# Kernel tuning notes

Hardware: AMD Instinct MI355X
Metric: run time of the kernel (lower is better)

## Reference

```python
import jax, jax.numpy as jnp
import numpy as np

N = 100000   # total atoms in batch of graphs
E = 400000   # directed edges
B = 1024     # graphs / proteins in batch
F_XD = 78    # atom feature dim
DIM = 32     # GIN hidden dim
OUT_DIM = 128
EMB = 128    # protein token embed dim
VOCAB = 26   # num_features_xt + 1
NF = 32      # conv1d filters
SEQ = 1000
K = 8        # conv1d kernel size
LM = 1024    # LM embedding dim
FLAT = NF * (SEQ - K + 1)  # 31776
COMB = 2 * OUT_DIM + 2 * LM  # 2304


def setup_inputs() -> dict:
    key = jax.random.key(0)
    ks = jax.random.split(key, 40)
    s = 0.05  # weight scale
    nrm = lambda k, shape: (jax.random.normal(k, shape, jnp.float32) * s)
    inp = {
        'x': jax.random.normal(ks[0], (N, F_XD), jnp.float32),
        'edge_index': jax.random.randint(ks[1], (2, E), 0, N),
        'batch': jnp.sort(jax.random.randint(ks[2], (N,), 0, B)),
        'target': jax.random.randint(ks[3], (B, SEQ), 0, VOCAB),
        'drug_lm': jax.random.normal(ks[4], (B, LM), jnp.float32),
        'protein_lm': jax.random.normal(ks[5], (B, LM), jnp.float32),
        # GINConv 1 MLP (78->32->32)
        'w1a': nrm(ks[6], (F_XD, DIM)), 'b1a': jnp.zeros((DIM,), jnp.float32),
        'w1b': nrm(ks[7], (DIM, DIM)), 'b1b': jnp.zeros((DIM,), jnp.float32),
        # GINConv 2-5 MLPs stacked (32->32->32)
        'gw_a': nrm(ks[8], (4, DIM, DIM)), 'gb_a': jnp.zeros((4, DIM), jnp.float32),
        'gw_b': nrm(ks[9], (4, DIM, DIM)), 'gb_b': jnp.zeros((4, DIM), jnp.float32),
        # BatchNorm affine params for 5 layers
        'bn_gamma': jnp.ones((5, DIM), jnp.float32),
        'bn_beta': jnp.zeros((5, DIM), jnp.float32),
        'fc1_xd_w': nrm(ks[10], (DIM, OUT_DIM)), 'fc1_xd_b': jnp.zeros((OUT_DIM,), jnp.float32),
        'emb': nrm(ks[11], (VOCAB, EMB)),
        'convxt_w': nrm(ks[12], (NF, EMB, K)), 'convxt_b': jnp.zeros((NF,), jnp.float32),
        'fc1_xt_w': nrm(ks[13], (FLAT, OUT_DIM)) * 0.1, 'fc1_xt_b': jnp.zeros((OUT_DIM,), jnp.float32),
        'fc1_w': nrm(ks[14], (COMB, 1024)), 'fc1_b': jnp.zeros((1024,), jnp.float32),
        'fc2_w': nrm(ks[15], (1024, 256)), 'fc2_b': jnp.zeros((256,), jnp.float32),
        'out_w': nrm(ks[16], (256, 1)), 'out_b': jnp.zeros((1,), jnp.float32),
    }
    return inp


def reference(x, edge_index, batch, target, drug_lm, protein_lm,
              w1a, b1a, w1b, b1b, gw_a, gb_a, gw_b, gb_b,
              bn_gamma, bn_beta, fc1_xd_w, fc1_xd_b, emb,
              convxt_w, convxt_b, fc1_xt_w, fc1_xt_b,
              fc1_w, fc1_b, fc2_w, fc2_b, out_w, out_b):
    src, dst = edge_index[0], edge_index[1]

    def bn(z, g, be):
        mu = z.mean(axis=0)
        var = jnp.mean((z - mu) ** 2, axis=0)
        return g * (z - mu) * jax.lax.rsqrt(var + 1e-5) + be

    def gin(h, wa, ba, wb, bb, g, be):
        # GIN aggregation: out_i = MLP((1+eps)*x_i + sum_{j->i} x_j), eps=0
        agg = jax.ops.segment_sum(h[src], dst, num_segments=N)
        z = jnp.maximum((h + agg) @ wa + ba, 0.0) @ wb + bb
        return bn(jnp.maximum(z, 0.0), g, be)  # relu then BatchNorm

    h = gin(x, w1a, b1a, w1b, b1b, bn_gamma[0], bn_beta[0])
    for i in range(4):  # convs 2..5
        h = gin(h, gw_a[i], gb_a[i], gw_b[i], gb_b[i], bn_gamma[i + 1], bn_beta[i + 1])

    xg = jax.ops.segment_sum(h, batch, num_segments=B)  # global_add_pool -> [B, 32]
    xg = jnp.maximum(xg @ fc1_xd_w + fc1_xd_b, 0.0)      # [B, 128]

    e = emb[target]                      # [B, SEQ, EMB]
    e = jnp.transpose(e, (0, 2, 1))      # [B, EMB, SEQ]
    c = jax.lax.conv_general_dilated(e, convxt_w, (1,), 'VALID',
                                     dimension_numbers=('NCH', 'OIH', 'NCH'))
    c = jnp.maximum(c + convxt_b[None, :, None], 0.0)    # [B, 32, 993]
    xt = jnp.maximum(c.reshape(B, -1) @ fc1_xt_w + fc1_xt_b, 0.0)  # [B, 128]

    xc = jnp.concatenate([xg, xt, drug_lm, protein_lm], axis=1)  # [B, 2304]
    xc = jnp.maximum(xc @ fc1_w + fc1_b, 0.0)
    xc = jnp.maximum(xc @ fc2_w + fc2_b, 0.0)
    return xc @ out_w + out_b  # [B, 1]
```

## Files before the change

### kernel.cpp

```cpp
#include <hip/hip_runtime.h>
#include <hip/hip_bf16.h>

#define NN 100000
#define EE 400000
#define BB 1024
#define FXD 78
#define DIMC 32
#define VOCABN 26
#define SEQN 1000
#define PCONV 993
#define FLATN 31776
#define COMB 2304
#define NB_SC 391

static __device__ __forceinline__ float relu_(float x) { return x > 0.f ? x : 0.f; }

template<int KC, bool TRANSFORM>
__global__ __launch_bounds__(256) void gin_gemm1(
    const float* __restrict__ H, const float* __restrict__ W, float* __restrict__ P,
    const float* __restrict__ sums, const float* __restrict__ gamma, const float* __restrict__ beta)
{
    __shared__ float As[32][KC + 1];
    __shared__ float Ws[KC][32];
    __shared__ float scale_s[32], shift_s[32];
    const int tid = threadIdx.x;
    const int row0 = blockIdx.x * 32;
    if (TRANSFORM) {
        if (tid < 32) {
            float mu = sums[tid] * (1.f / NN);
            float var = sums[32 + tid] * (1.f / NN) - mu * mu;
            float rs = rsqrtf(var + 1e-5f);
            float a = gamma[tid] * rs;
            scale_s[tid] = a;
            shift_s[tid] = beta[tid] - mu * a;
        }
    }
    for (int idx = tid; idx < KC * 32; idx += 256) Ws[idx / 32][idx % 32] = W[idx];
    __syncthreads();
    for (int idx = tid; idx < 32 * KC; idx += 256) {
        int r = idx / KC, k = idx % KC;
        float v = H[(row0 + r) * KC + k];
        if (TRANSFORM) v = v * scale_s[k] + shift_s[k];
        As[r][k] = v;
    }
    __syncthreads();
    const int col = tid & 31, rg = tid >> 5;
    float acc[4] = {0.f, 0.f, 0.f, 0.f};
    for (int k = 0; k < KC; ++k) {
        float w = Ws[k][col];
#pragma unroll
        for (int r = 0; r < 4; ++r) acc[r] += As[rg + 8 * r][k] * w;
    }
#pragma unroll
    for (int r = 0; r < 4; ++r) P[(row0 + rg + 8 * r) * 32 + col] = acc[r];
}

__global__ __launch_bounds__(256) void gin_gemm2(
    const float* __restrict__ P, const float* __restrict__ AGG, const float* __restrict__ W,
    const float* __restrict__ ba, const float* __restrict__ bb,
    float* __restrict__ Y, float* __restrict__ partials)
{
    __shared__ float As[32][33];
    __shared__ float Ws[32][32];
    __shared__ float red[8][32], red2[8][32];
    const int tid = threadIdx.x;
    const int row0 = blockIdx.x * 32;
    for (int idx = tid; idx < 1024; idx += 256) Ws[idx / 32][idx % 32] = W[idx];
    for (int idx = tid; idx < 1024; idx += 256) {
        int r = idx / 32, k = idx % 32;
        int g = (row0 + r) * 32 + k;
        As[r][k] = relu_(P[g] + AGG[g] + ba[k]);
    }
    __syncthreads();
    const int col = tid & 31, rg = tid >> 5;
    float acc[4] = {0.f, 0.f, 0.f, 0.f};
    for (int k = 0; k < 32; ++k) {
        float w = Ws[k][col];
#pragma unroll
        for (int r = 0; r < 4; ++r) acc[r] += As[rg + 8 * r][k] * w;
    }
    float s = 0.f, ss = 0.f;
#pragma unroll
    for (int r = 0; r < 4; ++r) {
        float y = relu_(acc[r] + bb[col]);
        Y[(row0 + rg + 8 * r) * 32 + col] = y;
        s += y; ss += y * y;
    }
    red[rg][col] = s; red2[rg][col] = ss;
    __syncthreads();
    if (tid < 32) {
        float t1 = 0.f, t2 = 0.f;
#pragma unroll
        for (int i = 0; i < 8; ++i) { t1 += red[i][tid]; t2 += red2[i][tid]; }
        partials[blockIdx.x * 64 + tid] = t1;
        partials[blockIdx.x * 64 + 32 + tid] = t2;
    }
}

__global__ __launch_bounds__(256) void hist_kernel(const int* __restrict__ dst, int* __restrict__ deg)
{
    int e = blockIdx.x * 256 + threadIdx.x;
    if (e < EE) atomicAdd(&deg[dst[e]], 1);
}

__global__ __launch_bounds__(256) void scan1_kernel(
    const int* __restrict__ deg, int* __restrict__ scanex, int* __restrict__ bsums)
{
    __shared__ int tmp[2][256];
    int tid = threadIdx.x, g = blockIdx.x * 256 + tid;
    int v = (g < NN) ? deg[g] : 0;
    tmp[0][tid] = v;
    __syncthreads();
    int cur = 0;
    for (int off = 1; off < 256; off <<= 1) {
        int nxt = cur ^ 1;
        tmp[nxt][tid] = tmp[cur][tid] + ((tid >= off) ? tmp[cur][tid - off] : 0);
        cur = nxt;
        __syncthreads();
    }
    int incl = tmp[cur][tid];
    if (g < NN) scanex[g] = incl - v;
    if (tid == 255) bsums[blockIdx.x] = incl;
}

__global__ __launch_bounds__(512) void scan2_kernel(const int* __restrict__ bsums, int* __restrict__ bexcl)
{
    __shared__ int tmp[2][512];
    int tid = threadIdx.x;
    int v = (tid < NB_SC) ? bsums[tid] : 0;
    tmp[0][tid] = v;
    __syncthreads();
    int cur = 0;
    for (int off = 1; off < 512; off <<= 1) {
        int nxt = cur ^ 1;
        tmp[nxt][tid] = tmp[cur][tid] + ((tid >= off) ? tmp[cur][tid - off] : 0);
        cur = nxt;
        __syncthreads();
    }
    if (tid < NB_SC) bexcl[tid] = tmp[cur][tid] - v;
}

__global__ __launch_bounds__(256) void rowptr_kernel(
    const int* __restrict__ scanex, const int* __restrict__ bexcl, int* __restrict__ rowptr)
{
    int g = blockIdx.x * 256 + threadIdx.x;
    if (g < NN) rowptr[g] = scanex[g] + bexcl[g >> 8];
    if (g == 0) rowptr[NN] = EE;
}

__global__ __launch_bounds__(256) void fill_kernel(
    const int* __restrict__ src, const int* __restrict__ dst,
    const int* __restrict__ rowptr, int* __restrict__ cursor, int* __restrict__ eidx)
{
    int e = blockIdx.x * 256 + threadIdx.x;
    if (e >= EE) return;
    int d = dst[e];
    int slot = rowptr[d] + atomicAdd(&cursor[d], 1);
    eidx[slot] = src[e];
}

__global__ __launch_bounds__(256) void gather_kernel(
    const int* __restrict__ rowptr, const int* __restrict__ eidx,
    const float* __restrict__ P, float* __restrict__ AGG)
{
    int t = blockIdx.x * 256 + threadIdx.x;
    int n = t >> 3, q = t & 7;
    if (n >= NN) return;
    int s = rowptr[n], e = rowptr[n + 1];
    float4 acc = make_float4(0.f, 0.f, 0.f, 0.f);
    for (int p = s; p < e; ++p) {
        int sn = eidx[p];
        float4 v = *(const float4*)&P[(size_t)sn * 32 + q * 4];
        acc.x += v.x; acc.y += v.y; acc.z += v.z; acc.w += v.w;
    }
    *(float4*)&AGG[(size_t)n * 32 + q * 4] = acc;
}

__global__ __launch_bounds__(256) void stat_reduce(const float* __restrict__ partials, float* __restrict__ sums)
{
    const int j = blockIdx.x;
    float s = 0.f;
    for (int i = threadIdx.x; i < 3125; i += 256) s += partials[i * 64 + j];
#pragma unroll
    for (int off = 32; off > 0; off >>= 1) s += __shfl_down(s, off);
    __shared__ float wsum[4];
    int w = threadIdx.x >> 6, lane = threadIdx.x & 63;
    if (lane == 0) wsum[w] = s;
    __syncthreads();
    if (threadIdx.x == 0) sums[j] = wsum[0] + wsum[1] + wsum[2] + wsum[3];
}

__global__ __launch_bounds__(256) void pool_kernel(
    const float* __restrict__ Y, const int* __restrict__ batch,
    const float* __restrict__ sums, const float* __restrict__ gamma, const float* __restrict__ beta,
    float* __restrict__ XG)
{
    __shared__ float scale_s[32], shift_s[32];
    int tid = threadIdx.x;
    if (tid < 32) {
        float mu = sums[tid] * (1.f / NN);
        float var = sums[32 + tid] * (1.f / NN) - mu * mu;
        float rs = rsqrtf(var + 1e-5f);
        float a = gamma[tid] * rs;
        scale_s[tid] = a; shift_s[tid] = beta[tid] - mu * a;
    }
    __syncthreads();
    int idx = blockIdx.x * 256 + tid;
    if (idx >= NN * 32) return;
    int i = idx >> 5, c = idx & 31;
    float v = Y[idx] * scale_s[c] + shift_s[c];
    atomicAdd(&XG[batch[i] * 32 + c], v);
}

__global__ __launch_bounds__(128) void fc_xd_kernel(
    const float* __restrict__ XG, const float* __restrict__ W, const float* __restrict__ b,
    float* __restrict__ XD)
{
    __shared__ float xs[32];
    int tid = threadIdx.x, blk = blockIdx.x;
    if (tid < 32) xs[tid] = XG[blk * 32 + tid];
    __syncthreads();
    float acc = b[tid];
    for (int k = 0; k < 32; ++k) acc += xs[k] * W[k * 128 + tid];
    XD[blk * 128 + tid] = relu_(acc);
}

__global__ __launch_bounds__(256) void mtable_kernel(
    const float* __restrict__ emb, const float* __restrict__ cw, float* __restrict__ M)
{
    int v = blockIdx.x, tid = threadIdx.x;
    int k = tid >> 5, f = tid & 31;
    float acc = 0.f;
    for (int c = 0; c < 128; ++c) acc += emb[v * 128 + c] * cw[f * 1024 + c * 8 + k];
    M[f * 208 + v * 8 + k] = acc;
}

__global__ __launch_bounds__(256) void xt_fused(
    const int* __restrict__ target, const float* __restrict__ M, const float* __restrict__ cb,
    const float* __restrict__ W, float* __restrict__ out)
{
    __shared__ float As[32][68];
    __shared__ float Ws[32][132];
    __shared__ int   toks[64][41];
    __shared__ float Ms[26 * 9];
    const int tid = threadIdx.x;
    const int m0 = blockIdx.x * 64;
    const int f  = blockIdx.z;
    const int tx = tid & 31, ty = tid >> 5;
    const float cbf = cb[f];

    for (int i = tid; i < 208; i += 256) Ms[(i >> 3) * 9 + (i & 7)] = M[f * 208 + i];
    __syncthreads();

    float4 acc[8];
#pragma unroll
    for (int i = 0; i < 8; ++i) acc[i] = make_float4(0.f, 0.f, 0.f, 0.f);

    for (int p0 = 0; p0 < PCONV; p0 += 32) {
#pragma unroll
        for (int t = 0; t < 10; ++t) {
            int idx = tid + t * 256;
            int r = idx / 40, c = idx - r * 40;
            int p = p0 + c;
            toks[r][c] = (p < SEQN) ? target[(size_t)(m0 + r) * SEQN + p] : 0;
        }
#pragma unroll
        for (int t = 0; t < 4; ++t) {
            int f4i = tid + t * 256;
            int kk = f4i >> 5, n4 = f4i & 31;
            float4 wv = make_float4(0.f, 0.f, 0.f, 0.f);
            if (p0 + kk < PCONV)
                wv = *(const float4*)&W[(size_t)(f * PCONV + p0 + kk) * 128 + 4 * n4];
            *(float4*)&Ws[kk][4 * n4] = wv;
        }
        __syncthreads();
#pragma unroll
        for (int t = 0; t < 8; ++t) {
            int idx = tid + t * 256;
            int r = idx & 63, kk = idx >> 6;
            int p = p0 + kk;
            float s = 0.f;
            if (p < PCONV) {
                s = cbf;
#pragma unroll
                for (int j = 0; j < 8; ++j)
                    s += Ms[toks[r][kk + j] * 9 + j];
                s = relu_(s);
            }
            As[kk][r] = s;
        }
        __syncthreads();
#pragma unroll
        for (int kk = 0; kk < 32; ++kk) {
            float4 wv = *(const float4*)&Ws[kk][4 * tx];
#pragma unroll
            for (int j = 0; j < 2; ++j) {
                float4 av = *(const float4*)&As[kk][8 * ty + 4 * j];
                float ar[4] = {av.x, av.y, av.z, av.w};
#pragma unroll
                for (int i = 0; i < 4; ++i) {
                    acc[4 * j + i].x += ar[i] * wv.x;
                    acc[4 * j + i].y += ar[i] * wv.y;
                    acc[4 * j + i].z += ar[i] * wv.z;
                    acc[4 * j + i].w += ar[i] * wv.w;
                }
            }
        }
        __syncthreads();
    }

    float* dst = out + (size_t)f * (size_t)(16 * 64) * 128;
#pragma unroll
    for (int i = 0; i < 8; ++i)
        *(float4*)&dst[(size_t)(m0 + 8 * ty + i) * 128 + 4 * tx] = acc[i];
}

template<int TN>
__global__ __launch_bounds__(256) void gemm_v3(
    const float* __restrict__ A, const float* __restrict__ W,
    float* __restrict__ out, int lda, int ldw, int ldo, int k_end, int k_chunk)
{
    constexpr int NG = TN / 4;
    constexpr int MR = NG / 4;
    __shared__ float As[32][64 + 4];
    __shared__ float Ws[32][TN + 4];
    const int tid = threadIdx.x;
    const int m0 = blockIdx.x * 64, n0 = blockIdx.y * TN;
    const int kb = blockIdx.z * k_chunk;
    const int ke = min(kb + k_chunk, k_end);
    const int tx = tid % NG, ty = tid / NG;

    float4 acc[MR];
#pragma unroll
    for (int i = 0; i < MR; ++i) acc[i] = make_float4(0.f, 0.f, 0.f, 0.f);

    const int nk = (ke - kb) >> 5;
    for (int kit = 0; kit < nk; ++kit) {
        const int k0 = kb + kit * 32;
#pragma unroll
        for (int t = 0; t < 2; ++t) {
            int f4i = tid + t * 256;
            int r = f4i >> 3, c = f4i & 7;
            float4 v = *(const float4*)&A[(size_t)(m0 + r) * lda + k0 + 4 * c];
            As[4 * c + 0][r] = v.x; As[4 * c + 1][r] = v.y;
            As[4 * c + 2][r] = v.z; As[4 * c + 3][r] = v.w;
        }
#pragma unroll
        for (int t = 0; t < NG / 8; ++t) {
            int f4i = tid + t * 256;
            int kk = f4i / NG, n4 = f4i % NG;
            *(float4*)&Ws[kk][4 * n4] = *(const float4*)&W[(size_t)(k0 + kk) * ldw + n0 + 4 * n4];
        }
        __syncthreads();
#pragma unroll
        for (int kk = 0; kk < 32; ++kk) {
            float4 wv = *(const float4*)&Ws[kk][4 * tx];
#pragma unroll
            for (int j = 0; j < MR / 4; ++j) {
                float4 av = *(const float4*)&As[kk][MR * ty + 4 * j];
                float ar[4] = {av.x, av.y, av.z, av.w};
#pragma unroll
                for (int i = 0; i < 4; ++i) {
                    acc[4 * j + i].x += ar[i] * wv.x;
                    acc[4 * j + i].y += ar[i] * wv.y;
                    acc[4 * j + i].z += ar[i] * wv.z;
                    acc[4 * j + i].w += ar[i] * wv.w;
                }
            }
        }
        __syncthreads();
    }
    for (int k = kb + nk * 32; k < ke; ++k) {
        float4 wv = *(const float4*)&W[(size_t)k * ldw + n0 + 4 * tx];
#pragma unroll
        for (int i = 0; i < MR; ++i) {
            float a = A[(size_t)(m0 + MR * ty + i) * lda + k];
            acc[i].x += a * wv.x; acc[i].y += a * wv.y;
            acc[i].z += a * wv.z; acc[i].w += a * wv.w;
        }
    }

    float* dst = out + (size_t)blockIdx.z * (size_t)(gridDim.x * 64) * (size_t)ldo;
#pragma unroll
    for (int i = 0; i < MR; ++i)
        *(float4*)&dst[(size_t)(m0 + MR * ty + i) * ldo + n0 + 4 * tx] = acc[i];
}

__global__ __launch_bounds__(256) void splitk_reduce(
    const float* __restrict__ part, const float* __restrict__ bias,
    float* __restrict__ out, int MN, int N, int nz)
{
    int i4 = blockIdx.x * 256 + threadIdx.x;
    size_t base = (size_t)i4 * 4;
    if (base >= (size_t)MN) return;
    float4 s = make_float4(0.f, 0.f, 0.f, 0.f);
    for (int z = 0; z < nz; ++z) {
        float4 p = *(const float4*)&part[(size_t)z * MN + base];
        s.x += p.x; s.y += p.y; s.z += p.z; s.w += p.w;
    }
    int n0 = (int)(base % (size_t)N);
    float4 b = *(const float4*)&bias[n0];
    s.x = relu_(s.x + b.x); s.y = relu_(s.y + b.y);
    s.z = relu_(s.z + b.z); s.w = relu_(s.w + b.w);
    *(float4*)&out[base] = s;
}

__global__ __launch_bounds__(256) void concat_kernel(
    const float* __restrict__ XD, const float* __restrict__ XT,
    const float* __restrict__ drug, const float* __restrict__ prot, float* __restrict__ XC)
{
    int idx = blockIdx.x * 256 + threadIdx.x;
    if (idx >= BB * COMB) return;
    int b = idx / COMB, j = idx - b * COMB;
    float v;
    if (j < 128) v = XD[b * 128 + j];
    else if (j < 256) v = XT[b * 128 + (j - 128)];
    else if (j < 1280) v = drug[b * 1024 + (j - 256)];
    else v = prot[b * 1024 + (j - 1280)];
    XC[idx] = v;
}

__global__ __launch_bounds__(256) void out_kernel(
    const float* __restrict__ X, const float* __restrict__ ow, const float* __restrict__ ob,
    float* __restrict__ out)
{
    int wv = threadIdx.x >> 6, lane = threadIdx.x & 63;
    int b = blockIdx.x * 4 + wv;
    float acc = 0.f;
#pragma unroll
    for (int t = 0; t < 4; ++t) {
        int j = lane + t * 64;
        acc += X[b * 256 + j] * ow[j];
    }
#pragma unroll
    for (int off = 32; off > 0; off >>= 1) acc += __shfl_down(acc, off);
    if (lane == 0) out[b] = acc + ob[0];
}

extern "C" void kernel_launch(void* const* d_in, const int* in_sizes, int n_in,
                              void* d_out, int out_size, void* d_ws, size_t ws_size,
                              hipStream_t stream)
{
    (void)in_sizes; (void)n_in; (void)out_size; (void)ws_size;
    const float* x          = (const float*)d_in[0];
    const int*   edge       = (const int*)d_in[1];
    const int*   batch      = (const int*)d_in[2];
    const int*   target     = (const int*)d_in[3];
    const float* drug_lm    = (const float*)d_in[4];
    const float* protein_lm = (const float*)d_in[5];
    const float* w1a        = (const float*)d_in[6];
    const float* b1a        = (const float*)d_in[7];
    const float* w1b        = (const float*)d_in[8];
    const float* b1b        = (const float*)d_in[9];
    const float* gw_a       = (const float*)d_in[10];
    const float* gb_a       = (const float*)d_in[11];
    const float* gw_b       = (const float*)d_in[12];
    const float* gb_b       = (const float*)d_in[13];
    const float* bn_gamma   = (const float*)d_in[14];
    const float* bn_beta    = (const float*)d_in[15];
    const float* fc1_xd_w   = (const float*)d_in[16];
    const float* fc1_xd_b   = (const float*)d_in[17];
    const float* emb        = (const float*)d_in[18];
    const float* convxt_w   = (const float*)d_in[19];
    const float* convxt_b   = (const float*)d_in[20];
    const float* fc1_xt_w   = (const float*)d_in[21];
    const float* fc1_xt_b   = (const float*)d_in[22];
    const float* fc1_w      = (const float*)d_in[23];
    const float* fc1_b      = (const float*)d_in[24];
    const float* fc2_w      = (const float*)d_in[25];
    const float* fc2_b      = (const float*)d_in[26];
    const float* out_w      = (const float*)d_in[27];
    const float* out_b      = (const float*)d_in[28];
    float* out = (float*)d_out;

    char* ws = (char*)d_ws;
    size_t off = 0;
    auto alloc = [&](size_t bytes) -> void* {
        void* p = ws + off;
        off = (off + bytes + 255) & ~(size_t)255;
        return p;
    };
    float* P        = (float*)alloc((size_t)NN * 32 * 4);
    float* AGG      = (float*)alloc((size_t)NN * 32 * 4);
    float* Y0       = (float*)alloc((size_t)NN * 32 * 4);
    float* Y1       = (float*)alloc((size_t)NN * 32 * 4);
    float* partials = (float*)alloc((size_t)3125 * 64 * 4);
    float* sums     = (float*)alloc(64 * 4);
    float* XG       = (float*)alloc((size_t)BB * 32 * 4);
    float* XD       = (float*)alloc((size_t)BB * 128 * 4);
    float* Mt       = (float*)alloc((size_t)26 * 256 * 4);
    float* XT       = (float*)alloc((size_t)BB * 128 * 4);
    float* XC       = (float*)alloc((size_t)BB * COMB * 4);
    float* XC2      = (float*)alloc((size_t)BB * 1024 * 4);
    float* XC3      = (float*)alloc((size_t)BB * 256 * 4);
    float* SCR      = (float*)alloc((size_t)80 * 1024 * 1024);

    float* xt_part  = P;
    float* fc1_part = SCR;
    float* fc2_part = SCR + (size_t)4 * 1024 * 1024;
    char*  csr      = (char*)SCR + (size_t)48 * 1024 * 1024;
    int* deg    = (int*)csr;
    int* cursor = deg + NN;
    int* scanex = cursor + NN;
    int* bsums  = scanex + NN;
    int* bexcl  = bsums + 512;
    int* rowptr = bexcl + 512;
    int* eidx   = rowptr + (NN + 2);

    const int* src = edge;
    const int* dst = edge + EE;

    mtable_kernel<<<26, 256, 0, stream>>>(emb, convxt_w, Mt);
    xt_fused<<<dim3(16, 1, 32), 256, 0, stream>>>(target, Mt, convxt_b, fc1_xt_w, xt_part);
    splitk_reduce<<<128, 256, 0, stream>>>(xt_part, fc1_xt_b, XT, BB * 128, 128, 32);

    hipMemsetAsync(deg, 0, (size_t)2 * NN * 4, stream);
    hist_kernel<<<1563, 256, 0, stream>>>(dst, deg);
    scan1_kernel<<<NB_SC, 256, 0, stream>>>(deg, scanex, bsums);
    scan2_kernel<<<1, 512, 0, stream>>>(bsums, bexcl);
    rowptr_kernel<<<NB_SC, 256, 0, stream>>>(scanex, bexcl, rowptr);
    fill_kernel<<<1563, 256, 0, stream>>>(src, dst, rowptr, cursor, eidx);

    gin_gemm1<78, false><<<3125, 256, 0, stream>>>(x, w1a, P, nullptr, nullptr, nullptr);
    gather_kernel<<<3125, 256, 0, stream>>>(rowptr, eidx, P, AGG);
    gin_gemm2<<<3125, 256, 0, stream>>>(P, AGG, w1b, b1a, b1b, Y0, partials);
    stat_reduce<<<64, 256, 0, stream>>>(partials, sums);

    float* yin = Y0; float* yout = Y1;
    for (int li = 0; li < 4; ++li) {
        gin_gemm1<32, true><<<3125, 256, 0, stream>>>(
            yin, gw_a + li * 1024, P, sums, bn_gamma + li * 32, bn_beta + li * 32);
        gather_kernel<<<3125, 256, 0, stream>>>(rowptr, eidx, P, AGG);
        gin_gemm2<<<3125, 256, 0, stream>>>(
            P, AGG, gw_b + li * 1024, gb_a + li * 32, gb_b + li * 32, yout, partials);
        stat_reduce<<<64, 256, 0, stream>>>(partials, sums);
        float* t = yin; yin = yout; yout = t;
    }

    hipMemsetAsync(XG, 0, (size_t)BB * 32 * 4, stream);
    pool_kernel<<<12500, 256, 0, stream>>>(yin, batch, sums, bn_gamma + 4 * 32, bn_beta + 4 * 32, XG);
    fc_xd_kernel<<<BB, 128, 0, stream>>>(XG, fc1_xd_w, fc1_xd_b, XD);

    concat_kernel<<<9216, 256, 0, stream>>>(XD, XT, drug_lm, protein_lm, XC);
    gemm_v3<128><<<dim3(16, 8, 4), 256, 0, stream>>>(
        XC, fc1_w, fc1_part, COMB, 1024, 1024, COMB, 576);
    splitk_reduce<<<1024, 256, 0, stream>>>(fc1_part, fc1_b, XC2, BB * 1024, 1024, 4);
    gemm_v3<128><<<dim3(16, 2, 8), 256, 0, stream>>>(
        XC2, fc2_w, fc2_part, 1024, 256, 256, 1024, 128);
    splitk_reduce<<<256, 256, 0, stream>>>(fc2_part, fc2_b, XC3, BB * 256, 256, 8);
    out_kernel<<<256, 256, 0, stream>>>(XC3, out_w, out_b, out);
}
```

Measured before the change: 865.3 us.

## Fuse neighbor gather into GIN second GEMM and split xt conv along sequence

Merges the CSR neighbor-gather into the second GIN GEMM kernel, so the aggregated features are built straight into shared memory instead of being written to and re-read from a global AGG buffer. This also drops five kernel launches. Separately, the fused conv+fc1_xt kernel now splits the 993 conv positions into two halves across the z grid dimension, which doubles the block count to improve occupancy, with the split-K reduce summing 64 partials. The cost is a larger partial buffer, and the gather now runs inside a GEMM block, so its irregular latency may stall that block.

```diff
diff --git a/kernel.cpp b/kernel.cpp
--- a/kernel.cpp
+++ b/kernel.cpp
@@ -55,8 +55,9 @@
     for (int r = 0; r < 4; ++r) P[(row0 + rg + 8 * r) * 32 + col] = acc[r];
 }
 
-__global__ __launch_bounds__(256) void gin_gemm2(
-    const float* __restrict__ P, const float* __restrict__ AGG, const float* __restrict__ W,
+__global__ __launch_bounds__(256) void gin_gather_gemm2(
+    const int* __restrict__ rowptr, const int* __restrict__ eidx,
+    const float* __restrict__ P, const float* __restrict__ W,
     const float* __restrict__ ba, const float* __restrict__ bb,
     float* __restrict__ Y, float* __restrict__ partials)
 {
@@ -66,10 +67,21 @@
     const int tid = threadIdx.x;
     const int row0 = blockIdx.x * 32;
     for (int idx = tid; idx < 1024; idx += 256) Ws[idx / 32][idx % 32] = W[idx];
-    for (int idx = tid; idx < 1024; idx += 256) {
-        int r = idx / 32, k = idx % 32;
-        int g = (row0 + r) * 32 + k;
-        As[r][k] = relu_(P[g] + AGG[g] + ba[k]);
+    {
+        int r = tid >> 3, q = tid & 7;
+        int n = row0 + r;
+        int s = rowptr[n], e = rowptr[n + 1];
+        float4 acc = *(const float4*)&P[(size_t)n * 32 + q * 4];
+        for (int p = s; p < e; ++p) {
+            int sn = eidx[p];
+            float4 v = *(const float4*)&P[(size_t)sn * 32 + q * 4];
+            acc.x += v.x; acc.y += v.y; acc.z += v.z; acc.w += v.w;
+        }
+        float4 bv = *(const float4*)&ba[q * 4];
+        As[r][4 * q + 0] = relu_(acc.x + bv.x);
+        As[r][4 * q + 1] = relu_(acc.y + bv.y);
+        As[r][4 * q + 2] = relu_(acc.z + bv.z);
+        As[r][4 * q + 3] = relu_(acc.w + bv.w);
     }
     __syncthreads();
     const int col = tid & 31, rg = tid >> 5;
@@ -157,23 +169,6 @@
     int d = dst[e];
     int slot = rowptr[d] + atomicAdd(&cursor[d], 1);
     eidx[slot] = src[e];
-}
-
-__global__ __launch_bounds__(256) void gather_kernel(
-    const int* __restrict__ rowptr, const int* __restrict__ eidx,
-    const float* __restrict__ P, float* __restrict__ AGG)
-{
-    int t = blockIdx.x * 256 + threadIdx.x;
-    int n = t >> 3, q = t & 7;
-    if (n >= NN) return;
-    int s = rowptr[n], e = rowptr[n + 1];
-    float4 acc = make_float4(0.f, 0.f, 0.f, 0.f);
-    for (int p = s; p < e; ++p) {
-        int sn = eidx[p];
-        float4 v = *(const float4*)&P[(size_t)sn * 32 + q * 4];
-        acc.x += v.x; acc.y += v.y; acc.z += v.z; acc.w += v.w;
-    }
-    *(float4*)&AGG[(size_t)n * 32 + q * 4] = acc;
 }
 
 __global__ __launch_bounds__(256) void stat_reduce(const float* __restrict__ partials, float* __restrict__ sums)
@@ -245,7 +240,10 @@
     __shared__ float Ms[26 * 9];
     const int tid = threadIdx.x;
     const int m0 = blockIdx.x * 64;
-    const int f  = blockIdx.z;
+    const int f  = blockIdx.z >> 1;
+    const int h  = blockIdx.z & 1;
+    const int pbase = h * 512;
+    const int pend  = min(pbase + 512, PCONV);
     const int tx = tid & 31, ty = tid >> 5;
     const float cbf = cb[f];
 
@@ -256,7 +254,7 @@
 #pragma unroll
     for (int i = 0; i < 8; ++i) acc[i] = make_float4(0.f, 0.f, 0.f, 0.f);
 
-    for (int p0 = 0; p0 < PCONV; p0 += 32) {
+    for (int p0 = pbase; p0 < pend; p0 += 32) {
 #pragma unroll
         for (int t = 0; t < 10; ++t) {
             int idx = tid + t * 256;
@@ -269,7 +267,7 @@
             int f4i = tid + t * 256;
             int kk = f4i >> 5, n4 = f4i & 31;
             float4 wv = make_float4(0.f, 0.f, 0.f, 0.f);
-            if (p0 + kk < PCONV)
+            if (p0 + kk < pend)
                 wv = *(const float4*)&W[(size_t)(f * PCONV + p0 + kk) * 128 + 4 * n4];
             *(float4*)&Ws[kk][4 * n4] = wv;
         }
@@ -280,7 +278,7 @@
             int r = idx & 63, kk = idx >> 6;
             int p = p0 + kk;
             float s = 0.f;
-            if (p < PCONV) {
+            if (p < pend) {
                 s = cbf;
 #pragma unroll
                 for (int j = 0; j < 8; ++j)
@@ -309,7 +307,7 @@
         __syncthreads();
     }
 
-    float* dst = out + (size_t)f * (size_t)(16 * 64) * 128;
+    float* dst = out + (size_t)blockIdx.z * (size_t)(16 * 64) * 128;
 #pragma unroll
     for (int i = 0; i < 8; ++i)
         *(float4*)&dst[(size_t)(m0 + 8 * ty + i) * 128 + 4 * tx] = acc[i];
@@ -511,8 +509,8 @@
     const int* dst = edge + EE;
 
     mtable_kernel<<<26, 256, 0, stream>>>(emb, convxt_w, Mt);
-    xt_fused<<<dim3(16, 1, 32), 256, 0, stream>>>(target, Mt, convxt_b, fc1_xt_w, xt_part);
-    splitk_reduce<<<128, 256, 0, stream>>>(xt_part, fc1_xt_b, XT, BB * 128, 128, 32);
+    xt_fused<<<dim3(16, 1, 64), 256, 0, stream>>>(target, Mt, convxt_b, fc1_xt_w, xt_part);
+    splitk_reduce<<<128, 256, 0, stream>>>(xt_part, fc1_xt_b, XT, BB * 128, 128, 64);
 
     hipMemsetAsync(deg, 0, (size_t)2 * NN * 4, stream);
     hist_kernel<<<1563, 256, 0, stream>>>(dst, deg);
@@ -522,17 +520,15 @@
     fill_kernel<<<1563, 256, 0, stream>>>(src, dst, rowptr, cursor, eidx);
 
     gin_gemm1<78, false><<<3125, 256, 0, stream>>>(x, w1a, P, nullptr, nullptr, nullptr);
-    gather_kernel<<<3125, 256, 0, stream>>>(rowptr, eidx, P, AGG);
-    gin_gemm2<<<3125, 256, 0, stream>>>(P, AGG, w1b, b1a, b1b, Y0, partials);
+    gin_gather_gemm2<<<3125, 256, 0, stream>>>(rowptr, eidx, P, w1b, b1a, b1b, Y0, partials);
     stat_reduce<<<64, 256, 0, stream>>>(partials, sums);
 
     float* yin = Y0; float* yout = Y1;
     for (int li = 0; li < 4; ++li) {
         gin_gemm1<32, true><<<3125, 256, 0, stream>>>(
             yin, gw_a + li * 1024, P, sums, bn_gamma + li * 32, bn_beta + li * 32);
-        gather_kernel<<<3125, 256, 0, stream>>>(rowptr, eidx, P, AGG);
-        gin_gemm2<<<3125, 256, 0, stream>>>(
-            P, AGG, gw_b + li * 1024, gb_a + li * 32, gb_b + li * 32, yout, partials);
+        gin_gather_gemm2<<<3125, 256, 0, stream>>>(
+            rowptr, eidx, P, gw_b + li * 1024, gb_a + li * 32, gb_b + li * 32, yout, partials);
         stat_reduce<<<64, 256, 0, stream>>>(partials, sums);
         float* t = yin; yin = yout; yout = t;
     }
```

New measurement: 841.7 us. -2.7%, faster.
